# Kernel optimization log

Hardware: AMD Instinct MI355X
Metric: run time of the kernel (lower is better)

Reference implementation:

```python
import jax, jax.numpy as jnp
import numpy as np


def setup_inputs() -> dict:
    key = jax.random.key(0)
    k0, k1, k2 = jax.random.split(key, 3)
    B, S, E, U = 32, 2048, 512, 512
    return {
        "seq": jax.random.normal(k0, (B, S, E), jnp.float32),
        "w1": jax.random.normal(k1, (U, E), jnp.float32) * 0.05,
        "b1": jnp.zeros((U,), jnp.float32),
        "w2": jax.random.normal(k2, (3, U), jnp.float32) * 0.05,
        "b2": jnp.zeros((3,), jnp.float32),
        "num_lists": 16,
        "list_size": 16,
    }


def reference(seq, w1, b1, w2, b2, num_lists, list_size):
    B, S, E = seq.shape
    # action decoder: Linear -> SiLU -> Linear -> Softmax over 3 actions
    h = jax.nn.silu(jnp.einsum('bse,ue->bsu', seq, w1) + b1)
    actions = jax.nn.softmax(jnp.einsum('bsu,au->bsa', h, w2) + b2, axis=-1)  # (B,S,3)

    Hn, Wn = num_lists, list_size
    T0 = jnp.zeros((B, Hn, Wn), seq.dtype).at[:, 0, -1].set(1.0)   # superposition grid
    rs0 = jnp.zeros((B, Hn), seq.dtype).at[:, 0].set(1.0)          # row sums

    # process actions in reverse token order; scan over seq dim
    acts_rev = jnp.swapaxes(actions[:, ::-1, :], 0, 1)  # (S,B,3)

    def step(carry, a):
        T, rs = carry
        a0, a1, a2 = a[:, 0:1], a[:, 1:2], a[:, 2:3]  # each (B,1)
        # weight used to place the current (reversed) token: (a0+a1)*T
        w_step = (a0 + a1)[:, :, None] * T  # (B,H,W)
        # devolve: the grouped conv2d with kernel [0, a2, a0] is a width-shift blend
        other = a2[:, :, None] * T[:, :, :-1] + a0[:, :, None] * T[:, :, 1:]  # cols 0..W-2
        sums = a1 * jnp.roll(rs, 1, axis=1).at[:, 0].set(0.0)                 # (B,H)
        last = sums + a2 * T[:, :, -1]                                        # (B,H)
        rs_new = (a0 + a2) * rs + sums
        T_new = jnp.concatenate([other, last[:, :, None]], axis=2)
        return (T_new, rs_new), w_step

    _, ws = jax.lax.scan(step, (T0, rs0), acts_rev)  # ws: (S,B,H,W), aligned with reversed seq
    # G = sum_i w_i[...,None] * token_i[:,None,None,:]
    G = jnp.einsum('sbhw,bse->bhwe', ws, seq[:, ::-1, :])
    return G
```

## Files before the change

### kernel.cpp

```cpp
#include <hip/hip_runtime.h>
#include <stdint.h>

#define S_LEN 2048
#define NB 32
#define NE 512
#define NU 512
#define NP 256

typedef __bf16 bf16;
typedef __bf16 bf16x8 __attribute__((ext_vector_type(8)));
typedef __bf16 bf16x4 __attribute__((ext_vector_type(4)));
typedef float f32x4 __attribute__((ext_vector_type(4)));
typedef float f32x8 __attribute__((ext_vector_type(8)));

__device__ __forceinline__ void gload16(const void* g, void* l) {
    __builtin_amdgcn_global_load_lds(
        (__attribute__((address_space(1))) void*)g,
        (__attribute__((address_space(3))) void*)l, 16, 0, 0);
}

__device__ __forceinline__ float dpp_shr1_z(float x) {
    return __builtin_bit_cast(float, __builtin_amdgcn_update_dpp(
        0, __builtin_bit_cast(int, x), 0x111, 0xF, 0xF, true));
}
__device__ __forceinline__ float dpp_shl1_z(float x) {
    return __builtin_bit_cast(float, __builtin_amdgcn_update_dpp(
        0, __builtin_bit_cast(int, x), 0x101, 0xF, 0xF, true));
}

__device__ __forceinline__ void stage_tile(const bf16* __restrict__ src, int SR,
                                           bf16* lds, int tid) {
#pragma unroll
    for (int rnd = 0; rnd < 2; ++rnd) {
        const int c = rnd * 256 + tid;
        const int row = c >> 2;
        const int q = (c & 3) ^ ((c >> 3) & 3);
        gload16(src + (size_t)row * SR + q * 8, lds + c * 8);
    }
}

__global__ __launch_bounds__(256) void k_wconv(
    const float* __restrict__ w1, bf16* __restrict__ wHi, bf16* __restrict__ wLo)
{
    const int i = (blockIdx.x * 256 + threadIdx.x) * 4;
    const float4 v = *(const float4*)(w1 + i);
    const float vv[4] = {v.x, v.y, v.z, v.w};
    bf16x4 oh, ol;
#pragma unroll
    for (int q = 0; q < 4; ++q) {
        const bf16 hb = (bf16)vv[q];
        oh[q] = hb;
        ol[q] = (bf16)(vv[q] - (float)hb);
    }
    *(bf16x4*)(wHi + i) = oh;
    *(bf16x4*)(wLo + i) = ol;
}

__global__ __launch_bounds__(256, 2) void k_gemm1(
    const float* __restrict__ seq,
    const bf16* __restrict__ w1H, const bf16* __restrict__ w1L,
    const float* __restrict__ b1v, const float* __restrict__ w2,
    const float* __restrict__ b2v, float* __restrict__ actions)
{
    __shared__ __align__(16) bf16 BhL[2][4096];
    __shared__ __align__(16) bf16 BlL[2][4096];
    __shared__ float red[2][2][4][4][4][3];
    const int tid = threadIdx.x;
    const int wid = tid >> 6;
    const int wm = wid >> 1, wu = wid & 1;
    const int lane = tid & 63;
    const int lr = lane & 15, lg = lane >> 4;
    const int m0 = blockIdx.x << 7;

    const float* ar[4];
#pragma unroll
    for (int i = 0; i < 4; ++i)
        ar[i] = seq + (size_t)(m0 + wm * 64 + i * 16 + lr) * NE + lg * 8;
    const int lbase = (wu * 64 + lr) * 64 + (lg ^ ((lr >> 1) & 3)) * 16;

    float plog[3][4][4];
#pragma unroll
    for (int a = 0; a < 3; ++a)
#pragma unroll
        for (int i = 0; i < 4; ++i)
#pragma unroll
            for (int q = 0; q < 4; ++q) plog[a][i][q] = 0.f;

    f32x4 acc[4][4];
    stage_tile(w1H, NE, BhL[0], tid);
    stage_tile(w1L, NE, BlL[0], tid);
    f32x8 AC[4], AN[4];
#pragma unroll
    for (int i = 0; i < 4; ++i) AC[i] = *(const f32x8*)(ar[i]);

#define G1_BODY(g, buf, Ac, An) do {                                          \
        __syncthreads();                                                      \
        if (((g) & 15) == 0) {                                                \
            _Pragma("unroll") for (int i = 0; i < 4; ++i)                     \
            _Pragma("unroll") for (int j = 0; j < 4; ++j)                     \
                acc[i][j] = (f32x4)(0.f);                                     \
        }                                                                     \
        bf16x8 bh[4], bl[4];                                                  \
        _Pragma("unroll") for (int j = 0; j < 4; ++j) {                       \
            bh[j] = *(const bf16x8*)((const char*)BhL[buf] + j * 1024 + lbase);\
            bl[j] = *(const bf16x8*)((const char*)BlL[buf] + j * 1024 + lbase);\
        }                                                                     \
        __syncthreads();                                                      \
        if ((g) < 63) {                                                       \
            const int gn = (g) + 1;                                           \
            const int u0n = (gn >> 4) << 7;                                   \
            const int k0n = (gn & 15) << 5;                                   \
            stage_tile(w1H + (size_t)u0n * NE + k0n, NE, BhL[(buf) ^ 1], tid);\
            stage_tile(w1L + (size_t)u0n * NE + k0n, NE, BlL[(buf) ^ 1], tid);\
            _Pragma("unroll") for (int i = 0; i < 4; ++i)                     \
                An[i] = *(const f32x8*)(ar[i] + k0n);                         \
        }                                                                     \
        bf16x8 Ah[4], Al[4];                                                  \
        _Pragma("unroll") for (int i = 0; i < 4; ++i)                         \
        _Pragma("unroll") for (int e = 0; e < 8; ++e) {                       \
            const bf16 hb = (bf16)Ac[i][e];                                   \
            Ah[i][e] = hb; Al[i][e] = (bf16)(Ac[i][e] - (float)hb);           \
        }                                                                     \
        _Pragma("unroll") for (int j = 0; j < 4; ++j)                         \
        _Pragma("unroll") for (int i = 0; i < 4; ++i) {                       \
            acc[i][j] = __builtin_amdgcn_mfma_f32_16x16x32_bf16(Ah[i], bh[j], acc[i][j], 0, 0, 0); \
            acc[i][j] = __builtin_amdgcn_mfma_f32_16x16x32_bf16(Ah[i], bl[j], acc[i][j], 0, 0, 0); \
            acc[i][j] = __builtin_amdgcn_mfma_f32_16x16x32_bf16(Al[i], bh[j], acc[i][j], 0, 0, 0); \
        }                                                                     \
        if (((g) & 15) == 15) {                                               \
            const int p = (g) >> 4;                                           \
            _Pragma("unroll") for (int j = 0; j < 4; ++j) {                   \
                const int col = p * 128 + wu * 64 + j * 16 + lr;              \
                const float b1c = b1v[col];                                   \
                const float w20 = w2[col], w21 = w2[NU + col], w22 = w2[2 * NU + col]; \
                _Pragma("unroll") for (int i = 0; i < 4; ++i)                 \
                _Pragma("unroll") for (int q = 0; q < 4; ++q) {               \
                    const float x = acc[i][j][q] + b1c;                       \
                    const float hg = x / (1.f + __expf(-x));                  \
                    plog[0][i][q] = fmaf(hg, w20, plog[0][i][q]);             \
                    plog[1][i][q] = fmaf(hg, w21, plog[1][i][q]);             \
                    plog[2][i][q] = fmaf(hg, w22, plog[2][i][q]);             \
                }                                                             \
            }                                                                 \
        }                                                                     \
    } while (0)

    for (int gg = 0; gg < 32; ++gg) {
        G1_BODY(2 * gg, 0, AC, AN);
        G1_BODY(2 * gg + 1, 1, AN, AC);
    }
#undef G1_BODY

#pragma unroll
    for (int m = 1; m < 16; m <<= 1) {
#pragma unroll
        for (int a = 0; a < 3; ++a)
#pragma unroll
            for (int i = 0; i < 4; ++i)
#pragma unroll
                for (int q = 0; q < 4; ++q)
                    plog[a][i][q] += __shfl_xor(plog[a][i][q], m);
    }
    if (lr == 0) {
#pragma unroll
        for (int a = 0; a < 3; ++a)
#pragma unroll
            for (int i = 0; i < 4; ++i)
#pragma unroll
                for (int q = 0; q < 4; ++q)
                    red[wu][wm][i][lg][q][a] = plog[a][i][q];
    }
    __syncthreads();
    if (tid < 128) {
        const int r = tid;
        const int wmr = r >> 6, ir = (r >> 4) & 3, lgr = (r >> 2) & 3, qr = r & 3;
        float l0 = b2v[0] + red[0][wmr][ir][lgr][qr][0] + red[1][wmr][ir][lgr][qr][0];
        float l1 = b2v[1] + red[0][wmr][ir][lgr][qr][1] + red[1][wmr][ir][lgr][qr][1];
        float l2 = b2v[2] + red[0][wmr][ir][lgr][qr][2] + red[1][wmr][ir][lgr][qr][2];
        const float mx = fmaxf(l0, fmaxf(l1, l2));
        const float e0 = __expf(l0 - mx), e1 = __expf(l1 - mx), e2 = __expf(l2 - mx);
        const float inv = 1.f / (e0 + e1 + e2);
        *(float4*)(actions + (size_t)(m0 + r) * 4) = make_float4(e0 * inv, e1 * inv, e2 * inv, 0.f);
    }
}

union SPMem {
    float tile[64][65];
    struct {
        float4 actbuf[3][256];
        float  sums[2][256][16];
    } s;
};

__device__ __forceinline__ void rs_chunk(const float4* __restrict__ pb,
                                         float* __restrict__ so,
                                         float& rs, int lane)
{
    for (int w = 0; w < 32; ++w) {
        const int rtop = 255 - w * 8;
        const float4 e0 = pb[rtop],     e1 = pb[rtop - 1];
        const float4 e2 = pb[rtop - 2], e3 = pb[rtop - 3];
        const float4 e4 = pb[rtop - 4], e5 = pb[rtop - 5];
        const float4 e6 = pb[rtop - 6], e7 = pb[rtop - 7];
#define RS_STEP(E, k) do {                                                    \
        const float rsp = dpp_shr1_z(rs);                                     \
        const float s = (E).y * rsp;                                          \
        if (lane < 16) so[(rtop - (k)) * 16 + lane] = s;                      \
        rs = fmaf((E).x + (E).z, rs, s);                                      \
    } while (0)
        RS_STEP(e0, 0); RS_STEP(e1, 1); RS_STEP(e2, 2); RS_STEP(e3, 3);
        RS_STEP(e4, 4); RS_STEP(e5, 5); RS_STEP(e6, 6); RS_STEP(e7, 7);
#undef RS_STEP
    }
}

__device__ __forceinline__ void t_chunk(const float4* __restrict__ lb,
                                        const float* __restrict__ sp,
                                        float& T, bf16* __restrict__ obp,
                                        int tbase0, int w15)
{
    for (int w = 0; w < 32; ++w) {
        const int rtop = 255 - w * 8;
        const int tglob = tbase0 + rtop - 7;
        const float4 av0 = lb[rtop],     av1 = lb[rtop - 1];
        const float4 av2 = lb[rtop - 2], av3 = lb[rtop - 3];
        const float4 av4 = lb[rtop - 4], av5 = lb[rtop - 5];
        const float4 av6 = lb[rtop - 6], av7 = lb[rtop - 7];
        const float su0 = sp[rtop * 16],       su1 = sp[(rtop - 1) * 16];
        const float su2 = sp[(rtop - 2) * 16], su3 = sp[(rtop - 3) * 16];
        const float su4 = sp[(rtop - 4) * 16], su5 = sp[(rtop - 5) * 16];
        const float su6 = sp[(rtop - 6) * 16], su7 = sp[(rtop - 7) * 16];
        bf16x8 fr;
#define T_STEP(Av, Su, fi) do {                                               \
        const float a0 = (Av).x, a1 = (Av).y, a2 = (Av).z;                    \
        fr[fi] = (bf16)((a0 + a1) * T);                                       \
        const float nT = dpp_shl1_z(T);                                       \
        const float contrib = w15 ? (Su) : a0 * nT;                           \
        T = fmaf(a2, T, contrib);                                             \
    } while (0)
        T_STEP(av0, su0, 7); T_STEP(av1, su1, 6);
        T_STEP(av2, su2, 5); T_STEP(av3, su3, 4);
        T_STEP(av4, su4, 3); T_STEP(av5, su5, 2);
        T_STEP(av6, su6, 1); T_STEP(av7, su7, 0);
#undef T_STEP
        *(bf16x8*)(obp + tglob) = fr;
    }
}

__global__ __launch_bounds__(320) void k_scan_prep(
    const float* __restrict__ actions, bf16* __restrict__ wsT,
    const float* __restrict__ seq, bf16* __restrict__ tHi)
{
    __shared__ SPMem sm;
    const int tid = threadIdx.x;
    if (blockIdx.x < 32) {
        const int b = blockIdx.x;
        const int wid = tid >> 6;
        const int lane = tid & 63;
        const float4* actb = (const float4*)actions + (size_t)b * S_LEN;

        float rs = (lane == 0) ? 1.f : 0.f;
        float T = (wid == 0 && lane == 15) ? 1.f : 0.f;
        const int w15 = ((lane & 15) == 15) ? 1 : 0;
        bf16* obp = wsT + ((size_t)b * NP + wid * 64 + lane) * S_LEN;

        if (wid < 4) {
            gload16(actb + 1792 + wid * 64 + lane, &sm.s.actbuf[0][wid * 64]);
            gload16(actb + 1536 + wid * 64 + lane, &sm.s.actbuf[1][wid * 64]);
            asm volatile("s_waitcnt vmcnt(0)" ::: "memory");
        }
        __syncthreads();
        if (wid == 4) rs_chunk(sm.s.actbuf[0], &sm.s.sums[0][0][0], rs, lane);
        __syncthreads();

        int bufT = 0, bufP = 1, bufL = 2;
        for (int c = 0; c < 8; ++c) {
            if (wid < 4) {
                if (c < 6)
                    gload16(actb + (1280 - c * 256) + wid * 64 + lane,
                            &sm.s.actbuf[bufL][wid * 64]);
                t_chunk(sm.s.actbuf[bufT],
                        &sm.s.sums[c & 1][0][wid * 4 + (lane >> 4)],
                        T, obp, 1792 - c * 256, w15);
                asm volatile("s_waitcnt vmcnt(0)" ::: "memory");
            } else {
                if (c < 7)
                    rs_chunk(sm.s.actbuf[bufP], &sm.s.sums[(c + 1) & 1][0][0], rs, lane);
            }
            __syncthreads();
            const int t = bufT; bufT = bufP; bufP = bufL; bufL = t;
        }
        return;
    }
    const int bid = blockIdx.x - 32;
    const int b = bid >> 8;
    const int r = bid & 255;
    const int s0 = (r & 31) << 6;
    const int e0 = (r >> 5) << 6;
    const int tx = tid & 15, ty = (tid & 255) >> 4;
    const float* src = seq + ((size_t)b * S_LEN + s0) * NE + e0;
    if (tid < 256) {
#pragma unroll
        for (int i = 0; i < 4; ++i) {
            const int row = ty + i * 16;
            const float4 v = *(const float4*)(src + (size_t)row * NE + tx * 4);
            sm.tile[row][tx * 4 + 0] = v.x; sm.tile[row][tx * 4 + 1] = v.y;
            sm.tile[row][tx * 4 + 2] = v.z; sm.tile[row][tx * 4 + 3] = v.w;
        }
    }
    __syncthreads();
    if (tid < 256) {
        const int sx = tid & 7, ey = tid >> 3;
#pragma unroll
        for (int jj = 0; jj < 2; ++jj) {
            const int er = ey + jj * 32;
            bf16x8 oh;
#pragma unroll
            for (int q = 0; q < 8; ++q) oh[q] = (bf16)sm.tile[sx * 8 + q][er];
            *(bf16x8*)(tHi + ((size_t)b * NE + e0 + er) * S_LEN + s0 + sx * 8) = oh;
        }
    }
}

__global__ __launch_bounds__(256, 2) void k_gemm2(
    const bf16* __restrict__ wsT, const bf16* __restrict__ seqtH,
    float* __restrict__ part)
{
    __shared__ __align__(16) bf16 AL[2][4096];
    __shared__ __align__(16) bf16 BL[2][4096];
    const int tid = threadIdx.x;
    const int wid = tid >> 6;
    const int lane = tid & 63;
    const int lr = lane & 15, lg = lane >> 4;
    const int bid = blockIdx.x;
    const int b = bid >> 4;
    const int sub = bid & 15;
    const int kc = sub >> 3;
    const int p0 = ((sub >> 2) & 1) << 7;
    const int e0 = (sub & 3) << 7;

    const bf16* Abase = wsT + ((size_t)b * NP + p0) * S_LEN + kc * 1024;
    const bf16* Bbase = seqtH + ((size_t)b * NE + e0) * S_LEN + kc * 1024;
    const int lroff = lr * 64 + (lg ^ ((lr >> 1) & 3)) * 16;

    f32x4 acc[2][8];
#pragma unroll
    for (int i = 0; i < 2; ++i)
#pragma unroll
        for (int j = 0; j < 8; ++j) acc[i][j] = (f32x4)(0.f);

    stage_tile(Abase, S_LEN, AL[0], tid);
    stage_tile(Bbase, S_LEN, BL[0], tid);

#define G2_BODY(kt, buf) do {                                                 \
        __syncthreads();                                                      \
        bf16x8 af[2], bfv[8];                                                 \
        _Pragma("unroll") for (int i = 0; i < 2; ++i)                         \
            af[i] = *(const bf16x8*)((const char*)AL[buf]                     \
                     + (wid * 32 + i * 16) * 64 + lroff);                     \
        _Pragma("unroll") for (int j = 0; j < 8; ++j)                         \
            bfv[j] = *(const bf16x8*)((const char*)BL[buf] + j * 1024 + lroff);\
        __syncthreads();                                                      \
        if ((kt) < 31) {                                                      \
            stage_tile(Abase + ((kt) + 1) * 32, S_LEN, AL[(buf) ^ 1], tid);   \
            stage_tile(Bbase + ((kt) + 1) * 32, S_LEN, BL[(buf) ^ 1], tid);   \
        }                                                                     \
        _Pragma("unroll") for (int j = 0; j < 8; ++j) {                       \
            acc[0][j] = __builtin_amdgcn_mfma_f32_16x16x32_bf16(af[0], bfv[j], acc[0][j], 0, 0, 0); \
            acc[1][j] = __builtin_amdgcn_mfma_f32_16x16x32_bf16(af[1], bfv[j], acc[1][j], 0, 0, 0); \
        }                                                                     \
    } while (0)

    for (int kk = 0; kk < 16; ++kk) {
        G2_BODY(2 * kk, 0);
        G2_BODY(2 * kk + 1, 1);
    }
#undef G2_BODY

    float* obp = part + (((size_t)kc * NB + b) * NP + p0 + wid * 32) * NE + e0;
#pragma unroll
    for (int i = 0; i < 2; ++i)
#pragma unroll
        for (int j = 0; j < 8; ++j)
#pragma unroll
            for (int q = 0; q < 4; ++q)
                obp[(size_t)(i * 16 + lg * 4 + q) * NE + j * 16 + lr] = acc[i][j][q];
}

__global__ __launch_bounds__(256) void k_gred(
    const float* __restrict__ part, float* __restrict__ outp)
{
    const size_t i = ((size_t)blockIdx.x * 256 + threadIdx.x) * 4;
    const float4 p0 = *(const float4*)(part + i);
    const float4 p1 = *(const float4*)(part + ((size_t)NB * NP * NE) + i);
    *(float4*)(outp + i) = make_float4(p0.x + p1.x, p0.y + p1.y,
                                       p0.z + p1.z, p0.w + p1.w);
}

extern "C" void kernel_launch(void* const* d_in, const int* in_sizes, int n_in,
                              void* d_out, int out_size, void* d_ws, size_t ws_size,
                              hipStream_t stream) {
    (void)in_sizes; (void)n_in; (void)out_size; (void)ws_size;
    const float* seq = (const float*)d_in[0];
    const float* w1  = (const float*)d_in[1];
    const float* b1  = (const float*)d_in[2];
    const float* w2  = (const float*)d_in[3];
    const float* b2  = (const float*)d_in[4];
    float* outp = (float*)d_out;

    char* ws = (char*)d_ws;
    bf16*  seqtH   = (bf16*)(ws);
    bf16*  wsT     = (bf16*)(ws + (64ull << 20));
    float* actions = (float*)(ws + (96ull << 20));
    bf16*  w1H     = (bf16*)(ws + (97ull << 20));
    bf16*  w1L     = (bf16*)(ws + (97ull << 20) + (512u << 10));
    float* part    = (float*)(ws + (98ull << 20));

    hipLaunchKernelGGL(k_wconv, dim3(256),  dim3(256), 0, stream, w1, w1H, w1L);
    hipLaunchKernelGGL(k_gemm1, dim3(512),  dim3(256), 0, stream,
                       seq, w1H, w1L, b1, w2, b2, actions);
    hipLaunchKernelGGL(k_scan_prep, dim3(32 + 8192), dim3(320), 0, stream,
                       actions, wsT, seq, seqtH);
    hipLaunchKernelGGL(k_gemm2, dim3(512),  dim3(256), 0, stream, wsT, seqtH, part);
    hipLaunchKernelGGL(k_gred,  dim3(4096), dim3(256), 0, stream, part, outp);
}
```

Baseline: 341.3 us.

## Split gemm1 over four U-quarters with partial logits and a finalize kernel

The first GEMM now launches 2048 blocks, each covering one 128-row M tile and one 128-wide quarter of the hidden dimension, instead of 512 blocks that each looped over all of U. Each block writes partial action logits, and a new small kernel sums the four partials, adds the bias and applies the softmax. Block IDs are remapped so the four U-quarters of one M tile land on the same XCD, which should let them share the seq rows in L2. The aim is more parallelism and better CU occupancy for the GEMM, at the cost of an extra launch, a partial-logit buffer round trip, and reading each seq tile four times.

```diff
diff --git a/kernel.cpp b/kernel.cpp
--- a/kernel.cpp
+++ b/kernel.cpp
@@ -60,58 +60,57 @@
     const float* __restrict__ seq,
     const bf16* __restrict__ w1H, const bf16* __restrict__ w1L,
     const float* __restrict__ b1v, const float* __restrict__ w2,
-    const float* __restrict__ b2v, float* __restrict__ actions)
+    float* __restrict__ plogit)
 {
     __shared__ __align__(16) bf16 BhL[2][4096];
     __shared__ __align__(16) bf16 BlL[2][4096];
-    __shared__ float red[2][2][4][4][4][3];
+    __shared__ float red[2][128][3];
     const int tid = threadIdx.x;
     const int wid = tid >> 6;
     const int wm = wid >> 1, wu = wid & 1;
     const int lane = tid & 63;
     const int lr = lane & 15, lg = lane >> 4;
-    const int m0 = blockIdx.x << 7;
+
+    const int bid = blockIdx.x;
+    const int xcd = bid & 7;
+    const int idx = bid >> 3;
+    const int mblk = xcd * 64 + (idx >> 2);
+    const int uq = idx & 3;
+    const int m0 = mblk << 7;
+    const int u0 = uq << 7;
 
     const float* ar[4];
 #pragma unroll
     for (int i = 0; i < 4; ++i)
         ar[i] = seq + (size_t)(m0 + wm * 64 + i * 16 + lr) * NE + lg * 8;
     const int lbase = (wu * 64 + lr) * 64 + (lg ^ ((lr >> 1) & 3)) * 16;
-
-    float plog[3][4][4];
-#pragma unroll
-    for (int a = 0; a < 3; ++a)
-#pragma unroll
-        for (int i = 0; i < 4; ++i)
-#pragma unroll
-            for (int q = 0; q < 4; ++q) plog[a][i][q] = 0.f;
+    const bf16* bH = w1H + (size_t)u0 * NE;
+    const bf16* bL = w1L + (size_t)u0 * NE;
 
     f32x4 acc[4][4];
-    stage_tile(w1H, NE, BhL[0], tid);
-    stage_tile(w1L, NE, BlL[0], tid);
+#pragma unroll
+    for (int i = 0; i < 4; ++i)
+#pragma unroll
+        for (int j = 0; j < 4; ++j) acc[i][j] = (f32x4)(0.f);
+
+    stage_tile(bH, NE, BhL[0], tid);
+    stage_tile(bL, NE, BlL[0], tid);
     f32x8 AC[4], AN[4];
 #pragma unroll
     for (int i = 0; i < 4; ++i) AC[i] = *(const f32x8*)(ar[i]);
 
-#define G1_BODY(g, buf, Ac, An) do {                                          \
+#define G1_BODY(kt, buf, Ac, An) do {                                         \
         __syncthreads();                                                      \
-        if (((g) & 15) == 0) {                                                \
-            _Pragma("unroll") for (int i = 0; i < 4; ++i)                     \
-            _Pragma("unroll") for (int j = 0; j < 4; ++j)                     \
-                acc[i][j] = (f32x4)(0.f);                                     \
-        }                                                                     \
         bf16x8 bh[4], bl[4];                                                  \
         _Pragma("unroll") for (int j = 0; j < 4; ++j) {                       \
             bh[j] = *(const bf16x8*)((const char*)BhL[buf] + j * 1024 + lbase);\
             bl[j] = *(const bf16x8*)((const char*)BlL[buf] + j * 1024 + lbase);\
         }                                                                     \
         __syncthreads();                                                      \
-        if ((g) < 63) {                                                       \
-            const int gn = (g) + 1;                                           \
-            const int u0n = (gn >> 4) << 7;                                   \
-            const int k0n = (gn & 15) << 5;                                   \
-            stage_tile(w1H + (size_t)u0n * NE + k0n, NE, BhL[(buf) ^ 1], tid);\
-            stage_tile(w1L + (size_t)u0n * NE + k0n, NE, BlL[(buf) ^ 1], tid);\
+        if ((kt) < 15) {                                                      \
+            const int k0n = ((kt) + 1) << 5;                                  \
+            stage_tile(bH + k0n, NE, BhL[(buf) ^ 1], tid);                    \
+            stage_tile(bL + k0n, NE, BlL[(buf) ^ 1], tid);                    \
             _Pragma("unroll") for (int i = 0; i < 4; ++i)                     \
                 An[i] = *(const f32x8*)(ar[i] + k0n);                         \
         }                                                                     \
@@ -127,30 +126,37 @@
             acc[i][j] = __builtin_amdgcn_mfma_f32_16x16x32_bf16(Ah[i], bl[j], acc[i][j], 0, 0, 0); \
             acc[i][j] = __builtin_amdgcn_mfma_f32_16x16x32_bf16(Al[i], bh[j], acc[i][j], 0, 0, 0); \
         }                                                                     \
-        if (((g) & 15) == 15) {                                               \
-            const int p = (g) >> 4;                                           \
-            _Pragma("unroll") for (int j = 0; j < 4; ++j) {                   \
-                const int col = p * 128 + wu * 64 + j * 16 + lr;              \
-                const float b1c = b1v[col];                                   \
-                const float w20 = w2[col], w21 = w2[NU + col], w22 = w2[2 * NU + col]; \
-                _Pragma("unroll") for (int i = 0; i < 4; ++i)                 \
-                _Pragma("unroll") for (int q = 0; q < 4; ++q) {               \
-                    const float x = acc[i][j][q] + b1c;                       \
-                    const float hg = x / (1.f + __expf(-x));                  \
-                    plog[0][i][q] = fmaf(hg, w20, plog[0][i][q]);             \
-                    plog[1][i][q] = fmaf(hg, w21, plog[1][i][q]);             \
-                    plog[2][i][q] = fmaf(hg, w22, plog[2][i][q]);             \
-                }                                                             \
-            }                                                                 \
-        }                                                                     \
     } while (0)
 
-    for (int gg = 0; gg < 32; ++gg) {
-        G1_BODY(2 * gg, 0, AC, AN);
-        G1_BODY(2 * gg + 1, 1, AN, AC);
+    for (int kk = 0; kk < 8; ++kk) {
+        G1_BODY(2 * kk, 0, AC, AN);
+        G1_BODY(2 * kk + 1, 1, AN, AC);
     }
 #undef G1_BODY
 
+    float plog[3][4][4];
+#pragma unroll
+    for (int a = 0; a < 3; ++a)
+#pragma unroll
+        for (int i = 0; i < 4; ++i)
+#pragma unroll
+            for (int q = 0; q < 4; ++q) plog[a][i][q] = 0.f;
+#pragma unroll
+    for (int j = 0; j < 4; ++j) {
+        const int col = u0 + wu * 64 + j * 16 + lr;
+        const float b1c = b1v[col];
+        const float w20 = w2[col], w21 = w2[NU + col], w22 = w2[2 * NU + col];
+#pragma unroll
+        for (int i = 0; i < 4; ++i)
+#pragma unroll
+            for (int q = 0; q < 4; ++q) {
+                const float x = acc[i][j][q] + b1c;
+                const float hg = x / (1.f + __expf(-x));
+                plog[0][i][q] = fmaf(hg, w20, plog[0][i][q]);
+                plog[1][i][q] = fmaf(hg, w21, plog[1][i][q]);
+                plog[2][i][q] = fmaf(hg, w22, plog[2][i][q]);
+            }
+    }
 #pragma unroll
     for (int m = 1; m < 16; m <<= 1) {
 #pragma unroll
@@ -163,25 +169,41 @@
     }
     if (lr == 0) {
 #pragma unroll
-        for (int a = 0; a < 3; ++a)
-#pragma unroll
-            for (int i = 0; i < 4; ++i)
-#pragma unroll
-                for (int q = 0; q < 4; ++q)
-                    red[wu][wm][i][lg][q][a] = plog[a][i][q];
+        for (int i = 0; i < 4; ++i)
+#pragma unroll
+            for (int q = 0; q < 4; ++q) {
+                const int rl = wm * 64 + i * 16 + lg * 4 + q;
+                red[wu][rl][0] = plog[0][i][q];
+                red[wu][rl][1] = plog[1][i][q];
+                red[wu][rl][2] = plog[2][i][q];
+            }
     }
     __syncthreads();
     if (tid < 128) {
-        const int r = tid;
-        const int wmr = r >> 6, ir = (r >> 4) & 3, lgr = (r >> 2) & 3, qr = r & 3;
-        float l0 = b2v[0] + red[0][wmr][ir][lgr][qr][0] + red[1][wmr][ir][lgr][qr][0];
-        float l1 = b2v[1] + red[0][wmr][ir][lgr][qr][1] + red[1][wmr][ir][lgr][qr][1];
-        float l2 = b2v[2] + red[0][wmr][ir][lgr][qr][2] + red[1][wmr][ir][lgr][qr][2];
-        const float mx = fmaxf(l0, fmaxf(l1, l2));
-        const float e0 = __expf(l0 - mx), e1 = __expf(l1 - mx), e2 = __expf(l2 - mx);
-        const float inv = 1.f / (e0 + e1 + e2);
-        *(float4*)(actions + (size_t)(m0 + r) * 4) = make_float4(e0 * inv, e1 * inv, e2 * inv, 0.f);
-    }
+        const float l0 = red[0][tid][0] + red[1][tid][0];
+        const float l1 = red[0][tid][1] + red[1][tid][1];
+        const float l2 = red[0][tid][2] + red[1][tid][2];
+        *(float4*)(plogit + ((size_t)(m0 + tid) * 4 + (size_t)uq * (size_t)NB * S_LEN * 4)) =
+            make_float4(l0, l1, l2, 0.f);
+    }
+}
+
+__global__ __launch_bounds__(256) void k_actfin(
+    const float* __restrict__ plogit, const float* __restrict__ b2v,
+    float* __restrict__ actions)
+{
+    const size_t row = (size_t)blockIdx.x * 256 + threadIdx.x;
+    const size_t stride = (size_t)NB * S_LEN * 4;
+    float l0 = b2v[0], l1 = b2v[1], l2 = b2v[2];
+#pragma unroll
+    for (int uq = 0; uq < 4; ++uq) {
+        const float4 p = *(const float4*)(plogit + row * 4 + uq * stride);
+        l0 += p.x; l1 += p.y; l2 += p.z;
+    }
+    const float mx = fmaxf(l0, fmaxf(l1, l2));
+    const float e0 = __expf(l0 - mx), e1 = __expf(l1 - mx), e2 = __expf(l2 - mx);
+    const float inv = 1.f / (e0 + e1 + e2);
+    *(float4*)(actions + row * 4) = make_float4(e0 * inv, e1 * inv, e2 * inv, 0.f);
 }
 
 union SPMem {
@@ -415,10 +437,13 @@
     bf16*  w1H     = (bf16*)(ws + (97ull << 20));
     bf16*  w1L     = (bf16*)(ws + (97ull << 20) + (512u << 10));
     float* part    = (float*)(ws + (98ull << 20));
+    float* plogit  = (float*)(ws + (130ull << 20));
 
     hipLaunchKernelGGL(k_wconv, dim3(256),  dim3(256), 0, stream, w1, w1H, w1L);
-    hipLaunchKernelGGL(k_gemm1, dim3(512),  dim3(256), 0, stream,
-                       seq, w1H, w1L, b1, w2, b2, actions);
+    hipLaunchKernelGGL(k_gemm1, dim3(2048), dim3(256), 0, stream,
+                       seq, w1H, w1L, b1, w2, plogit);
+    hipLaunchKernelGGL(k_actfin, dim3(256), dim3(256), 0, stream,
+                       plogit, b2, actions);
     hipLaunchKernelGGL(k_scan_prep, dim3(32 + 8192), dim3(320), 0, stream,
                        actions, wsT, seq, seqtH);
     hipLaunchKernelGGL(k_gemm2, dim3(512),  dim3(256), 0, stream, wsT, seqtH, part);
```

Measured after the change: 339.0 us. Within noise of the previous version (-0.7%).
